# Performance work log

Hardware: AMD Instinct MI355X
Metric: run time of the kernel (lower is better)

The kernel has to match this reference:

```python
import jax, jax.numpy as jnp
import numpy as np

N_VOX = 500000
P, S, K = 2048, 64, 8          # pixels(rays), samples per ray, voxel neighbors per sample
F_M, F_H = 64, 128             # voxel feature dim, mlp hidden dim
FREQ_PE = 4
DEPTH_MIN, DEPTH_MAX = 1.0, 80.0
RAY_SAMPLE_STEPS = 64.0
EPS = 1e-10
IN_FEAT = F_M + 3 * FREQ_PE * 2  # 88


def lrelu(x):
    return jnp.where(x >= 0, x, 0.1 * x)  # LeakyReLU(0.1)


def posenc(x, L=FREQ_PE):
    # NeRF positional encoding: sin/cos(2^i * x), i in [0, L)
    freqs = 2.0 ** jnp.arange(L, dtype=x.dtype)          # [L]
    ang = x[..., None] * freqs                            # [..., 3, L]
    enc = jnp.concatenate([jnp.sin(ang), jnp.cos(ang)], axis=-1)  # [..., 3, 2L]
    return enc.reshape(x.shape[:-1] + (x.shape[-1] * 2 * L,))


def setup_inputs() -> dict:
    key = jax.random.key(0)
    ks = jax.random.split(key, 16)

    def xavier(k, fan_in, fan_out):
        return jax.random.normal(k, (fan_in, fan_out), jnp.float32) / np.sqrt(fan_in)

    inp = {
        'map_xyz': jax.random.normal(ks[0], (N_VOX, 3), jnp.float32),
        'map_feat': jax.random.normal(ks[1], (N_VOX, F_M), jnp.float32) * 0.05,
        'ind_voxel': jax.random.randint(ks[2], (P, S, K), 0, N_VOX),
        'sample_xyz': jax.random.normal(ks[3], (P, S, 3), jnp.float32),
        'dist_to_cam': jax.random.uniform(ks[4], (P, S), jnp.float32) * RAY_SAMPLE_STEPS,
        'W0': xavier(ks[5], IN_FEAT, F_H), 'b0': jnp.full((F_H,), 0.01, jnp.float32),
        'W1': xavier(ks[6], F_H, F_H),     'b1': jnp.full((F_H,), 0.01, jnp.float32),
        'W2': xavier(ks[7], F_H, F_H),     'b2': jnp.full((F_H,), 0.01, jnp.float32),
        'Wa0': xavier(ks[8], F_H, F_H // 2), 'ba0': jnp.full((F_H // 2,), 0.01, jnp.float32),
        'Wa1': xavier(ks[9], F_H // 2, 1),   'ba1': jnp.full((1,), 0.01, jnp.float32),
        'Wr0': xavier(ks[10], F_H, F_H // 2), 'br0': jnp.full((F_H // 2,), 0.01, jnp.float32),
        'Wr1': xavier(ks[11], F_H // 2, 3),   'br1': jnp.full((3,), 0.01, jnp.float32),
    }
    return inp


def reference(map_xyz, map_feat, ind_voxel, sample_xyz, dist_to_cam,
              W0, b0, W1, b1, W2, b2, Wa0, ba0, Wa1, ba1, Wr0, br0, Wr1, br1):
    # ---- voxel -> sample messages (func_msg_voxel_to_sample) ----
    voxel_xyz = map_xyz[ind_voxel]                       # [P,S,K,3] gather
    feat = map_feat[ind_voxel]                           # [P,S,K,F_M] gather
    offset = sample_xyz[:, :, None, :] - voxel_xyz       # [P,S,K,3]
    h = jnp.concatenate([feat, posenc(offset)], axis=-1) # [P,S,K,88]
    h = lrelu(h @ W0 + b0)
    h = lrelu(h @ W1 + b1)
    h = lrelu(h @ W2 + b2)                               # [P,S,K,F_H]
    w = jnp.exp(-10.0 * jnp.linalg.norm(offset, axis=-1))  # [P,S,K]
    w = w / jnp.sum(w, axis=-1, keepdims=True)
    # ---- reduce over K neighbors (func_reduce_voxel_to_sample) ----
    feat_s = jnp.sum(h * w[..., None], axis=2)           # [P,S,F_H]
    a = lrelu(feat_s @ Wa0 + ba0)
    alpha = jax.nn.sigmoid(a @ Wa1 + ba1)                # [P,S,1]
    r = lrelu(feat_s @ Wr0 + br0)
    rgb = jax.nn.sigmoid(r @ Wr1 + br1)                  # [P,S,3]
    # ---- sample -> pixel volume rendering (func_reduce_sample_to_pixel) ----
    dist = DEPTH_MIN + DEPTH_MAX * dist_to_cam / RAY_SAMPLE_STEPS  # [P,S]
    ones = jnp.ones((P, 1, 1), alpha.dtype)
    trans = jnp.cumprod(jnp.concatenate([ones, 1.0 - alpha + EPS], axis=1), axis=1)[:, :-1, :]
    blend = alpha * trans                                # [P,S,1]
    pixel_rgb = jnp.sum(rgb * blend, axis=1)             # [P,3]
    pixel_d = jnp.sum(dist[..., None] * blend, axis=1)   # [P,1]
    acc = jnp.sum(blend, axis=1)                         # [P,1]
    return jnp.concatenate([pixel_rgb, pixel_d, acc], axis=-1)  # [P,5]
```

## Files before the change

kernel.cpp:

```cpp
#include <hip/hip_runtime.h>

typedef __bf16 bf16_t;
typedef __bf16 bf16x2 __attribute__((ext_vector_type(2)));
typedef __bf16 bf16x4 __attribute__((ext_vector_type(4)));
typedef __bf16 bf16x8 __attribute__((ext_vector_type(8)));
typedef float  f32x4  __attribute__((ext_vector_type(4)));

#define NPIX 2048
#define NS   64
#define NK   8
#define NSAMP (NPIX*NS)
#define NROWS (NSAMP*NK)
#define TROWS 64
#define NTILES (NROWS/TROWS)
#define XSTR 104
#define HSTR 136

#define PK_W0 0
#define PK_W1 1536
#define PK_W2 3584
#define PK_WA 5632
#define PK_WR 6656
#define PK_TOT 7680

#define WS_AR_BYTES 122880

__global__ void pack_weights(const float* __restrict__ W0, const float* __restrict__ W1,
                             const float* __restrict__ W2, const float* __restrict__ Wa0,
                             const float* __restrict__ Wr0, bf16_t* __restrict__ dst0) {
  int tid = blockIdx.x * blockDim.x + threadIdx.x;
  if (tid >= PK_TOT * 8) return;
  const float* src; bf16_t* dst; int e, KD, ND, KS;
  if (tid < 12288)      { src = W0;  dst = dst0;         e = tid;         KD = 88;  ND = 128; KS = 3; }
  else if (tid < 28672) { src = W1;  dst = dst0 + 12288; e = tid - 12288; KD = 128; ND = 128; KS = 4; }
  else if (tid < 45056) { src = W2;  dst = dst0 + 28672; e = tid - 28672; KD = 128; ND = 128; KS = 4; }
  else if (tid < 53248) { src = Wa0; dst = dst0 + 45056; e = tid - 45056; KD = 128; ND = 64;  KS = 4; }
  else                  { src = Wr0; dst = dst0 + 53248; e = tid - 53248; KD = 128; ND = 64;  KS = 4; }
  int j = e & 7, l = (e >> 3) & 63, f = e >> 9;
  int s = f % KS, t = f / KS;
  int row = s * 32 + (l >> 4) * 8 + j;
  int col = t * 16 + (l & 15);
  float v = (row < KD) ? src[row * ND + col] : 0.f;
  dst[e] = (bf16_t)v;
}

__device__ __forceinline__ float lrelu(float v) { return fmaxf(v, 0.1f * v); }
__device__ __forceinline__ float sigmoidf(float x) { return 1.f / (1.f + __expf(-x)); }

__global__ __launch_bounds__(512, 4)
void nerf_main(const float* __restrict__ map_xyz, const float* __restrict__ map_feat,
               const int* __restrict__ ind, const float* __restrict__ sample_xyz,
               const float* __restrict__ b0g, const float* __restrict__ b1g,
               const float* __restrict__ b2g, const float* __restrict__ ba0g,
               const float* __restrict__ wa1g, const float* __restrict__ ba1g,
               const float* __restrict__ br0g, const float* __restrict__ wr1g,
               const float* __restrict__ br1g, const bf16_t* __restrict__ wpack,
               float* __restrict__ ar_out)
{
  __shared__ __align__(16) bf16_t sBuf[TROWS * HSTR];
  __shared__ __align__(16) bf16_t sHa[TROWS * HSTR];
  __shared__ __align__(16) bf16_t sFS[16 * HSTR];
  __shared__ __align__(16) bf16_t sAR[16 * HSTR];
  __shared__ __align__(16) bf16_t sFB[2048];
  __shared__ __align__(16) float sWt[TROWS];
  __shared__ float sWs[8];
  __shared__ __align__(16) float sB0[128], sB1[128], sB2[128], sBH[128], sFBv[4];

  const int tid = threadIdx.x;
  const int wid = tid >> 6, l = tid & 63;
  const int q = l >> 4, n = l & 15;
  const int sr = tid >> 3, sp = tid & 7;

  const bf16x8* pk = (const bf16x8*)wpack;
  bf16x8 w0f[3], w1f[4], w2f[4], hdf[4];
#pragma unroll
  for (int s = 0; s < 3; s++) w0f[s] = pk[PK_W0 + (wid * 3 + s) * 64 + l];
#pragma unroll
  for (int s = 0; s < 4; s++) w1f[s] = pk[PK_W1 + (wid * 4 + s) * 64 + l];
#pragma unroll
  for (int s = 0; s < 4; s++) w2f[s] = pk[PK_W2 + (wid * 4 + s) * 64 + l];
#pragma unroll
  for (int s = 0; s < 4; s++)
    hdf[s] = pk[(wid < 4 ? PK_WA : PK_WR) + ((wid & 3) * 4 + s) * 64 + l];

  for (int i = tid; i < 8 * HSTR; i += 512) {
    sFS[8 * HSTR + i] = (bf16_t)0.f;
    sAR[8 * HSTR + i] = (bf16_t)0.f;
  }
  {
    int e0 = tid * 4;
    int jb = e0 & 7, ll = (e0 >> 3) & 63, s = e0 >> 9;
    int m = ll & 15;
#pragma unroll
    for (int ii = 0; ii < 4; ii++) {
      int k = s * 32 + (ll >> 4) * 8 + jb + ii;
      float v = 0.f;
      if (k < 64)  { if (m < 3) v = wr1g[k * 3 + m]; }
      else         { if (m == 3) v = wa1g[k - 64]; }
      sFB[e0 + ii] = (bf16_t)v;
    }
  }
  if (tid < 128)      sB0[tid] = b0g[tid];
  else if (tid < 256) sB1[tid - 128] = b1g[tid - 128];
  else if (tid < 384) sB2[tid - 256] = b2g[tid - 256];
  else { int t = tid - 384; sBH[t] = (t < 64) ? ba0g[t] : br0g[t - 64]; }
  if (tid < 4) sFBv[tid] = (tid < 3) ? br1g[tid] : ba1g[0];
  __syncthreads();

  int   pidx = 0;
  float4 pf0 = {}, pf1 = {};
  float ps0 = 0.f, ps1 = 0.f, ps2 = 0.f, pm0 = 0.f, pm1 = 0.f, pm2 = 0.f;

  auto prefetch = [&](int t) {
    const int m = t * TROWS + sr;
    pidx = ind[m];
    const float4* fp = (const float4*)(map_feat + (size_t)pidx * 64 + sp * 8);
    pf0 = fp[0]; pf1 = fp[1];
    const int g = m >> 3;
    if (sp < 6) {
      const int d = sp >> 1;
      ps0 = sample_xyz[g * 3 + d];
      pm0 = map_xyz[pidx * 3 + d];
    } else if (sp == 7) {
      ps0 = sample_xyz[g * 3 + 0]; pm0 = map_xyz[pidx * 3 + 0];
      ps1 = sample_xyz[g * 3 + 1]; pm1 = map_xyz[pidx * 3 + 1];
      ps2 = sample_xyz[g * 3 + 2]; pm2 = map_xyz[pidx * 3 + 2];
    }
  };

  prefetch(blockIdx.x);

  for (int tile = blockIdx.x; tile < NTILES; tile += gridDim.x) {
    const int m0 = tile * TROWS;

    {
      bf16x8 v;
      v[0] = (bf16_t)pf0.x; v[1] = (bf16_t)pf0.y; v[2] = (bf16_t)pf0.z; v[3] = (bf16_t)pf0.w;
      v[4] = (bf16_t)pf1.x; v[5] = (bf16_t)pf1.y; v[6] = (bf16_t)pf1.z; v[7] = (bf16_t)pf1.w;
      *(bf16x8*)(sBuf + sr * XSTR + sp * 8) = v;
      if (sp < 6) {
        const int d = sp >> 1;
        float o = ps0 - pm0;
        float s1 = __sinf(o), c1 = __cosf(o);
        float s2 = 2.f * s1 * c1, c2 = 1.f - 2.f * s1 * s1;
        float s4 = 2.f * s2 * c2, c4 = 1.f - 2.f * s2 * s2;
        float s8 = 2.f * s4 * c4, c8 = 1.f - 2.f * s4 * s4;
        bf16x4 e;
        if (sp & 1) { e[0] = (bf16_t)c1; e[1] = (bf16_t)c2; e[2] = (bf16_t)c4; e[3] = (bf16_t)c8; }
        else        { e[0] = (bf16_t)s1; e[1] = (bf16_t)s2; e[2] = (bf16_t)s4; e[3] = (bf16_t)s8; }
        *(bf16x4*)(sBuf + sr * XSTR + 64 + d * 8 + (sp & 1) * 4) = e;
      } else if (sp == 6) {
        bf16x8 z = {};
        *(bf16x8*)(sBuf + sr * XSTR + 88) = z;
      } else {
        float ox = ps0 - pm0, oy = ps1 - pm1, oz = ps2 - pm2;
        sWt[sr] = __expf(-10.f * sqrtf(ox * ox + oy * oy + oz * oz));
      }
    }
    __syncthreads();

    {
      int nt = tile + (int)gridDim.x;
      if (nt < NTILES) prefetch(nt);
    }

    if (tid < 8) {
      float ss = 0.f;
#pragma unroll
      for (int k = 0; k < 8; k++) ss += sWt[tid * 8 + k];
      sWs[tid] = ss;
    }

    {
      f32x4 b0i = *(const f32x4*)(sB0 + wid * 16 + q * 4);
      f32x4 acc[4] = {b0i, b0i, b0i, b0i};
      __builtin_amdgcn_s_setprio(1);
#pragma unroll
      for (int st = 0; st < 4; st++)
#pragma unroll
        for (int s = 0; s < 3; s++) {
          bf16x8 b = *(const bf16x8*)(sBuf + (st * 16 + n) * XSTR + s * 32 + q * 8);
          acc[st] = __builtin_amdgcn_mfma_f32_16x16x32_bf16(w0f[s], b, acc[st], 0, 0, 0);
        }
      __builtin_amdgcn_s_setprio(0);
#pragma unroll
      for (int st = 0; st < 4; st++) {
        bf16x4 o;
        o[0] = (bf16_t)lrelu(acc[st][0]);
        o[1] = (bf16_t)lrelu(acc[st][1]);
        o[2] = (bf16_t)lrelu(acc[st][2]);
        o[3] = (bf16_t)lrelu(acc[st][3]);
        *(bf16x4*)(sHa + (st * 16 + n) * HSTR + wid * 16 + q * 4) = o;
      }
    }
    __syncthreads();

    {
      f32x4 b1i = *(const f32x4*)(sB1 + wid * 16 + q * 4);
      f32x4 acc[4] = {b1i, b1i, b1i, b1i};
      __builtin_amdgcn_s_setprio(1);
#pragma unroll
      for (int st = 0; st < 4; st++)
#pragma unroll
        for (int s = 0; s < 4; s++) {
          bf16x8 b = *(const bf16x8*)(sHa + (st * 16 + n) * HSTR + s * 32 + q * 8);
          acc[st] = __builtin_amdgcn_mfma_f32_16x16x32_bf16(w1f[s], b, acc[st], 0, 0, 0);
        }
      __builtin_amdgcn_s_setprio(0);
#pragma unroll
      for (int st = 0; st < 4; st++) {
        bf16x4 o;
        o[0] = (bf16_t)lrelu(acc[st][0]);
        o[1] = (bf16_t)lrelu(acc[st][1]);
        o[2] = (bf16_t)lrelu(acc[st][2]);
        o[3] = (bf16_t)lrelu(acc[st][3]);
        *(bf16x4*)(sBuf + (st * 16 + n) * HSTR + wid * 16 + q * 4) = o;
      }
    }
    __syncthreads();

    {
      f32x4 b2i = *(const f32x4*)(sB2 + wid * 16 + q * 4);
      f32x4 acc[4] = {b2i, b2i, b2i, b2i};
      __builtin_amdgcn_s_setprio(1);
#pragma unroll
      for (int st = 0; st < 4; st++)
#pragma unroll
        for (int s = 0; s < 4; s++) {
          bf16x8 b = *(const bf16x8*)(sBuf + (st * 16 + n) * HSTR + s * 32 + q * 8);
          acc[st] = __builtin_amdgcn_mfma_f32_16x16x32_bf16(w2f[s], b, acc[st], 0, 0, 0);
        }
      __builtin_amdgcn_s_setprio(0);
#pragma unroll
      for (int st = 0; st < 4; st++) {
        bf16x4 o;
        o[0] = (bf16_t)lrelu(acc[st][0]);
        o[1] = (bf16_t)lrelu(acc[st][1]);
        o[2] = (bf16_t)lrelu(acc[st][2]);
        o[3] = (bf16_t)lrelu(acc[st][3]);
        *(bf16x4*)(sHa + (st * 16 + n) * HSTR + wid * 16 + q * 4) = o;
      }
    }
    __syncthreads();

    {
      int g = tid >> 6;
      int c = (tid & 63) * 2;
      float a0 = 0.f, a1 = 0.f;
#pragma unroll
      for (int k = 0; k < 8; k++) {
        float wk = sWt[g * 8 + k];
        unsigned u = *(const unsigned*)(sHa + (g * 8 + k) * HSTR + c);
        a0 += wk * __uint_as_float(u << 16);
        a1 += wk * __uint_as_float(u & 0xffff0000u);
      }
      float inv = 1.f / sWs[g];
      bf16x2 fo;
      fo[0] = (bf16_t)(a0 * inv);
      fo[1] = (bf16_t)(a1 * inv);
      *(bf16x2*)(sFS + g * HSTR + c) = fo;
    }
    __syncthreads();

    {
      f32x4 ha = *(const f32x4*)(sBH + wid * 16 + q * 4);
      __builtin_amdgcn_s_setprio(1);
#pragma unroll
      for (int s = 0; s < 4; s++) {
        bf16x8 b = *(const bf16x8*)(sFS + n * HSTR + s * 32 + q * 8);
        ha = __builtin_amdgcn_mfma_f32_16x16x32_bf16(hdf[s], b, ha, 0, 0, 0);
      }
      __builtin_amdgcn_s_setprio(0);
      if (n < 8) {
        const int base = (wid < 4) ? 64 : 0;
        bf16x4 o;
        o[0] = (bf16_t)lrelu(ha[0]);
        o[1] = (bf16_t)lrelu(ha[1]);
        o[2] = (bf16_t)lrelu(ha[2]);
        o[3] = (bf16_t)lrelu(ha[3]);
        *(bf16x4*)(sAR + n * HSTR + base + (wid & 3) * 16 + q * 4) = o;
      }
    }
    __syncthreads();

    if (wid == 0) {
      f32x4 c = *(const f32x4*)sFBv;
#pragma unroll
      for (int s = 0; s < 4; s++) {
        bf16x8 a = *(const bf16x8*)(sFB + (s * 64 + l) * 8);
        bf16x8 b = *(const bf16x8*)(sAR + n * HSTR + s * 32 + q * 8);
        c = __builtin_amdgcn_mfma_f32_16x16x32_bf16(a, b, c, 0, 0, 0);
      }
      if (q == 0 && n < 8) {
        float4 o;
        o.x = sigmoidf(c[0]);
        o.y = sigmoidf(c[1]);
        o.z = sigmoidf(c[2]);
        o.w = sigmoidf(c[3]);
        ((float4*)ar_out)[m0 / 8 + n] = o;
      }
    }
  }
}

__global__ __launch_bounds__(512)
void render_kernel(const float* __restrict__ ar, const float* __restrict__ dcam,
                   float* __restrict__ out) {
  int ray = blockIdx.x * 8 + (threadIdx.x >> 6);
  int s = threadIdx.x & 63;
  float4 v = ((const float4*)ar)[ray * 64 + s];
  float alpha = v.w;
  float t = 1.f - alpha + 1e-10f;
  float p = t;
#pragma unroll
  for (int d = 1; d < 64; d <<= 1) {
    float o = __shfl_up(p, d);
    if (s >= d) p *= o;
  }
  float pm1 = __shfl_up(p, 1);
  float T = (s == 0) ? 1.f : pm1;
  float bl = alpha * T;
  float dist = 1.f + 1.25f * dcam[ray * 64 + s];
  float cr = v.x * bl, cg = v.y * bl, cb = v.z * bl, cd = dist * bl, ca = bl;
#pragma unroll
  for (int d = 32; d > 0; d >>= 1) {
    cr += __shfl_xor(cr, d);
    cg += __shfl_xor(cg, d);
    cb += __shfl_xor(cb, d);
    cd += __shfl_xor(cd, d);
    ca += __shfl_xor(ca, d);
  }
  if (s == 0) {
    out[ray * 5 + 0] = cr; out[ray * 5 + 1] = cg; out[ray * 5 + 2] = cb;
    out[ray * 5 + 3] = cd; out[ray * 5 + 4] = ca;
  }
}

extern "C" void kernel_launch(void* const* d_in, const int* in_sizes, int n_in,
                              void* d_out, int out_size, void* d_ws, size_t ws_size,
                              hipStream_t stream) {
  const float* map_xyz    = (const float*)d_in[0];
  const float* map_feat   = (const float*)d_in[1];
  const int*   ind        = (const int*)d_in[2];
  const float* sample_xyz = (const float*)d_in[3];
  const float* dist_cam   = (const float*)d_in[4];
  const float* W0  = (const float*)d_in[5];
  const float* b0  = (const float*)d_in[6];
  const float* W1  = (const float*)d_in[7];
  const float* b1  = (const float*)d_in[8];
  const float* W2  = (const float*)d_in[9];
  const float* b2  = (const float*)d_in[10];
  const float* Wa0 = (const float*)d_in[11];
  const float* ba0 = (const float*)d_in[12];
  const float* Wa1 = (const float*)d_in[13];
  const float* ba1 = (const float*)d_in[14];
  const float* Wr0 = (const float*)d_in[15];
  const float* br0 = (const float*)d_in[16];
  const float* Wr1 = (const float*)d_in[17];
  const float* br1 = (const float*)d_in[18];

  bf16_t* wpack = (bf16_t*)d_ws;
  float*  ar    = (float*)((char*)d_ws + WS_AR_BYTES);

  pack_weights<<<240, 256, 0, stream>>>(W0, W1, W2, Wa0, Wr0, wpack);
  nerf_main<<<512, 512, 0, stream>>>(map_xyz, map_feat, ind, sample_xyz,
                                     b0, b1, b2, ba0, Wa1, ba1, br0, Wr1, br1,
                                     wpack, ar);
  render_kernel<<<256, 512, 0, stream>>>(ar, dist_cam, (float*)d_out);
}
```

Measured before the change: 409.9 us.

## Prefetch gathered voxel features directly into LDS with async global_load_lds

Replaces the register-held prefetch of the next tile's voxel features and coordinates with global_load_lds writes into new swizzled LDS buffers (sFeat, sVxyz, sSxyz). The index loads are issued early in the loop and the DMA-style copies after the barrier, so the gathers overlap with the MLP compute without occupying VGPRs. The cost is about 17 KB of extra LDS per block, which may limit occupancy. The LDS write ordering also relies on later barriers and the implicit vmcnt waits being correct.

```diff
diff --git a/kernel.cpp b/kernel.cpp
--- a/kernel.cpp
+++ b/kernel.cpp
@@ -24,6 +24,10 @@
 #define PK_TOT 7680
 
 #define WS_AR_BYTES 122880
+
+#define GLDS16(g, s) __builtin_amdgcn_global_load_lds(                          \
+    (const __attribute__((address_space(1))) void*)(g),                         \
+    (__attribute__((address_space(3))) void*)(s), 16, 0, 0)
 
 __global__ void pack_weights(const float* __restrict__ W0, const float* __restrict__ W1,
                              const float* __restrict__ W2, const float* __restrict__ Wa0,
@@ -65,6 +69,9 @@
   __shared__ __align__(16) float sWt[TROWS];
   __shared__ float sWs[8];
   __shared__ __align__(16) float sB0[128], sB1[128], sB2[128], sBH[128], sFBv[4];
+  __shared__ __align__(16) float sFeat[64 * 64];
+  __shared__ __align__(16) float sVxyz[64 * 4];
+  __shared__ __align__(16) float sSxyz[32];
 
   const int tid = threadIdx.x;
   const int wid = tid >> 6, l = tid & 63;
@@ -82,6 +89,24 @@
 #pragma unroll
   for (int s = 0; s < 4; s++)
     hdf[s] = pk[(wid < 4 ? PK_WA : PK_WR) + ((wid & 3) * 4 + s) * 64 + l];
+
+  int pidxA = 0, pidxB = 0, pidxC = 0;
+  float sampv = 0.f;
+  auto issueA = [&](int nt) {
+    const int m0n = nt * TROWS;
+    pidxA = ind[m0n + wid * 8 + (l >> 4)];
+    pidxB = ind[m0n + wid * 8 + 4 + (l >> 4)];
+    if (wid == 0) pidxC = ind[m0n + l];
+    if (wid == 1 && l < 24) sampv = sample_xyz[nt * 24 + l];
+  };
+  auto issueB = [&]() {
+    const int ca = (l & 15) ^ (l >> 4);
+    const int cb = (l & 15) ^ (4 | (l >> 4));
+    GLDS16(map_feat + (size_t)pidxA * 64 + ca * 4, sFeat + wid * 512);
+    GLDS16(map_feat + (size_t)pidxB * 64 + cb * 4, sFeat + wid * 512 + 256);
+    if (wid == 0) GLDS16(map_xyz + (size_t)pidxC * 3, sVxyz);
+    if (wid == 1 && l < 24) sSxyz[l] = sampv;
+  };
 
   for (int i = tid; i < 8 * HSTR; i += 512) {
     sFS[8 * HSTR + i] = (bf16_t)0.f;
@@ -105,42 +130,29 @@
   else if (tid < 384) sB2[tid - 256] = b2g[tid - 256];
   else { int t = tid - 384; sBH[t] = (t < 64) ? ba0g[t] : br0g[t - 64]; }
   if (tid < 4) sFBv[tid] = (tid < 3) ? br1g[tid] : ba1g[0];
+
+  issueA(blockIdx.x);
+  issueB();
   __syncthreads();
-
-  int   pidx = 0;
-  float4 pf0 = {}, pf1 = {};
-  float ps0 = 0.f, ps1 = 0.f, ps2 = 0.f, pm0 = 0.f, pm1 = 0.f, pm2 = 0.f;
-
-  auto prefetch = [&](int t) {
-    const int m = t * TROWS + sr;
-    pidx = ind[m];
-    const float4* fp = (const float4*)(map_feat + (size_t)pidx * 64 + sp * 8);
-    pf0 = fp[0]; pf1 = fp[1];
-    const int g = m >> 3;
-    if (sp < 6) {
-      const int d = sp >> 1;
-      ps0 = sample_xyz[g * 3 + d];
-      pm0 = map_xyz[pidx * 3 + d];
-    } else if (sp == 7) {
-      ps0 = sample_xyz[g * 3 + 0]; pm0 = map_xyz[pidx * 3 + 0];
-      ps1 = sample_xyz[g * 3 + 1]; pm1 = map_xyz[pidx * 3 + 1];
-      ps2 = sample_xyz[g * 3 + 2]; pm2 = map_xyz[pidx * 3 + 2];
-    }
-  };
-
-  prefetch(blockIdx.x);
 
   for (int tile = blockIdx.x; tile < NTILES; tile += gridDim.x) {
     const int m0 = tile * TROWS;
-
-    {
+    const int nt = tile + (int)gridDim.x;
+
+    if (nt < NTILES) issueA(nt);
+
+    {
+      const int sw = sr & 7;
+      const float* fb = sFeat + sr * 64;
+      f32x4 lo = *(const f32x4*)(fb + (((2 * sp)     ^ sw) << 2));
+      f32x4 hi = *(const f32x4*)(fb + (((2 * sp + 1) ^ sw) << 2));
       bf16x8 v;
-      v[0] = (bf16_t)pf0.x; v[1] = (bf16_t)pf0.y; v[2] = (bf16_t)pf0.z; v[3] = (bf16_t)pf0.w;
-      v[4] = (bf16_t)pf1.x; v[5] = (bf16_t)pf1.y; v[6] = (bf16_t)pf1.z; v[7] = (bf16_t)pf1.w;
+      v[0] = (bf16_t)lo[0]; v[1] = (bf16_t)lo[1]; v[2] = (bf16_t)lo[2]; v[3] = (bf16_t)lo[3];
+      v[4] = (bf16_t)hi[0]; v[5] = (bf16_t)hi[1]; v[6] = (bf16_t)hi[2]; v[7] = (bf16_t)hi[3];
       *(bf16x8*)(sBuf + sr * XSTR + sp * 8) = v;
       if (sp < 6) {
         const int d = sp >> 1;
-        float o = ps0 - pm0;
+        float o = sSxyz[(sr >> 3) * 3 + d] - sVxyz[sr * 4 + d];
         float s1 = __sinf(o), c1 = __cosf(o);
         float s2 = 2.f * s1 * c1, c2 = 1.f - 2.f * s1 * s1;
         float s4 = 2.f * s2 * c2, c4 = 1.f - 2.f * s2 * s2;
@@ -153,16 +165,15 @@
         bf16x8 z = {};
         *(bf16x8*)(sBuf + sr * XSTR + 88) = z;
       } else {
-        float ox = ps0 - pm0, oy = ps1 - pm1, oz = ps2 - pm2;
+        float ox = sSxyz[(sr >> 3) * 3 + 0] - sVxyz[sr * 4 + 0];
+        float oy = sSxyz[(sr >> 3) * 3 + 1] - sVxyz[sr * 4 + 1];
+        float oz = sSxyz[(sr >> 3) * 3 + 2] - sVxyz[sr * 4 + 2];
         sWt[sr] = __expf(-10.f * sqrtf(ox * ox + oy * oy + oz * oz));
       }
     }
     __syncthreads();
 
-    {
-      int nt = tile + (int)gridDim.x;
-      if (nt < NTILES) prefetch(nt);
-    }
+    if (nt < NTILES) issueB();
 
     if (tid < 8) {
       float ss = 0.f;
```

Result: faster. 396.5 us (-3.3%).

## Software-pipeline two tiles per iteration to interleave MLP stages and cut barriers

Applied to the files above, without the earlier changes.

The per-block tile loop is restructured so two tiles (A and B) are in flight at once: gather/encode, layer 0, layers 1 and 2, the K-reduction, the heads and the final outputs of one tile run in the same barrier phase as different stages of the other tile. This cuts the number of block-wide barriers per tile and lets MFMA work overlap the global gathers. The old register prefetch of the next tile's features is dropped; gathers are now issued inline and hidden only by the other tile's compute. Grid size and iteration count are hard-coded, and the extra LDS buffers raise shared-memory use per block, which may lower occupancy.

```diff
diff --git a/kernel.cpp b/kernel.cpp
--- a/kernel.cpp
+++ b/kernel.cpp
@@ -13,6 +13,8 @@
 #define NROWS (NSAMP*NK)
 #define TROWS 64
 #define NTILES (NROWS/TROWS)
+#define GRID   512
+#define NIT    16
 #define XSTR 104
 #define HSTR 136
 
@@ -57,13 +59,14 @@
                const float* __restrict__ br1g, const bf16_t* __restrict__ wpack,
                float* __restrict__ ar_out)
 {
-  __shared__ __align__(16) bf16_t sBuf[TROWS * HSTR];
-  __shared__ __align__(16) bf16_t sHa[TROWS * HSTR];
+  __shared__ __align__(16) bf16_t sH0[TROWS * HSTR];
+  __shared__ __align__(16) bf16_t sH1[TROWS * HSTR];
+  __shared__ __align__(16) bf16_t sX[TROWS * XSTR];
   __shared__ __align__(16) bf16_t sFS[16 * HSTR];
   __shared__ __align__(16) bf16_t sAR[16 * HSTR];
   __shared__ __align__(16) bf16_t sFB[2048];
-  __shared__ __align__(16) float sWt[TROWS];
-  __shared__ float sWs[8];
+  __shared__ __align__(16) float sWtA[TROWS], sWtB[TROWS];
+  __shared__ float sWsA[8], sWsB[8];
   __shared__ __align__(16) float sB0[128], sB1[128], sB2[128], sBH[128], sFBv[4];
 
   const int tid = threadIdx.x;
@@ -83,206 +86,123 @@
   for (int s = 0; s < 4; s++)
     hdf[s] = pk[(wid < 4 ? PK_WA : PK_WR) + ((wid & 3) * 4 + s) * 64 + l];
 
-  for (int i = tid; i < 8 * HSTR; i += 512) {
-    sFS[8 * HSTR + i] = (bf16_t)0.f;
-    sAR[8 * HSTR + i] = (bf16_t)0.f;
-  }
-  {
-    int e0 = tid * 4;
-    int jb = e0 & 7, ll = (e0 >> 3) & 63, s = e0 >> 9;
-    int m = ll & 15;
-#pragma unroll
-    for (int ii = 0; ii < 4; ii++) {
-      int k = s * 32 + (ll >> 4) * 8 + jb + ii;
-      float v = 0.f;
-      if (k < 64)  { if (m < 3) v = wr1g[k * 3 + m]; }
-      else         { if (m == 3) v = wa1g[k - 64]; }
-      sFB[e0 + ii] = (bf16_t)v;
-    }
-  }
-  if (tid < 128)      sB0[tid] = b0g[tid];
-  else if (tid < 256) sB1[tid - 128] = b1g[tid - 128];
-  else if (tid < 384) sB2[tid - 256] = b2g[tid - 256];
-  else { int t = tid - 384; sBH[t] = (t < 64) ? ba0g[t] : br0g[t - 64]; }
-  if (tid < 4) sFBv[tid] = (tid < 3) ? br1g[tid] : ba1g[0];
-  __syncthreads();
-
-  int   pidx = 0;
-  float4 pf0 = {}, pf1 = {};
-  float ps0 = 0.f, ps1 = 0.f, ps2 = 0.f, pm0 = 0.f, pm1 = 0.f, pm2 = 0.f;
-
-  auto prefetch = [&](int t) {
-    const int m = t * TROWS + sr;
-    pidx = ind[m];
-    const float4* fp = (const float4*)(map_feat + (size_t)pidx * 64 + sp * 8);
-    pf0 = fp[0]; pf1 = fp[1];
+  auto COMMIT = [&](int tile, bf16_t* X, float* wtbuf) {
+    const int m = tile * TROWS + sr;
+    const int idx = ind[m];
+    const float4* fp = (const float4*)(map_feat + (size_t)idx * 64 + sp * 8);
+    float4 f0 = fp[0], f1 = fp[1];
+    bf16x8 v;
+    v[0] = (bf16_t)f0.x; v[1] = (bf16_t)f0.y; v[2] = (bf16_t)f0.z; v[3] = (bf16_t)f0.w;
+    v[4] = (bf16_t)f1.x; v[5] = (bf16_t)f1.y; v[6] = (bf16_t)f1.z; v[7] = (bf16_t)f1.w;
+    *(bf16x8*)(X + sr * XSTR + sp * 8) = v;
     const int g = m >> 3;
     if (sp < 6) {
       const int d = sp >> 1;
-      ps0 = sample_xyz[g * 3 + d];
-      pm0 = map_xyz[pidx * 3 + d];
-    } else if (sp == 7) {
-      ps0 = sample_xyz[g * 3 + 0]; pm0 = map_xyz[pidx * 3 + 0];
-      ps1 = sample_xyz[g * 3 + 1]; pm1 = map_xyz[pidx * 3 + 1];
-      ps2 = sample_xyz[g * 3 + 2]; pm2 = map_xyz[pidx * 3 + 2];
-    }
-  };
-
-  prefetch(blockIdx.x);
-
-  for (int tile = blockIdx.x; tile < NTILES; tile += gridDim.x) {
-    const int m0 = tile * TROWS;
-
-    {
-      bf16x8 v;
-      v[0] = (bf16_t)pf0.x; v[1] = (bf16_t)pf0.y; v[2] = (bf16_t)pf0.z; v[3] = (bf16_t)pf0.w;
-      v[4] = (bf16_t)pf1.x; v[5] = (bf16_t)pf1.y; v[6] = (bf16_t)pf1.z; v[7] = (bf16_t)pf1.w;
-      *(bf16x8*)(sBuf + sr * XSTR + sp * 8) = v;
-      if (sp < 6) {
-        const int d = sp >> 1;
-        float o = ps0 - pm0;
-        float s1 = __sinf(o), c1 = __cosf(o);
-        float s2 = 2.f * s1 * c1, c2 = 1.f - 2.f * s1 * s1;
-        float s4 = 2.f * s2 * c2, c4 = 1.f - 2.f * s2 * s2;
-        float s8 = 2.f * s4 * c4, c8 = 1.f - 2.f * s4 * s4;
-        bf16x4 e;
-        if (sp & 1) { e[0] = (bf16_t)c1; e[1] = (bf16_t)c2; e[2] = (bf16_t)c4; e[3] = (bf16_t)c8; }
-        else        { e[0] = (bf16_t)s1; e[1] = (bf16_t)s2; e[2] = (bf16_t)s4; e[3] = (bf16_t)s8; }
-        *(bf16x4*)(sBuf + sr * XSTR + 64 + d * 8 + (sp & 1) * 4) = e;
-      } else if (sp == 6) {
-        bf16x8 z = {};
-        *(bf16x8*)(sBuf + sr * XSTR + 88) = z;
-      } else {
-        float ox = ps0 - pm0, oy = ps1 - pm1, oz = ps2 - pm2;
-        sWt[sr] = __expf(-10.f * sqrtf(ox * ox + oy * oy + oz * oz));
+      float o = sample_xyz[g * 3 + d] - map_xyz[idx * 3 + d];
+      float s1 = __sinf(o), c1 = __cosf(o);
+      float s2 = 2.f * s1 * c1, c2 = 1.f - 2.f * s1 * s1;
+      float s4 = 2.f * s2 * c2, c4 = 1.f - 2.f * s2 * s2;
+      float s8 = 2.f * s4 * c4, c8 = 1.f - 2.f * s4 * s4;
+      bf16x4 e;
+      if (sp & 1) { e[0] = (bf16_t)c1; e[1] = (bf16_t)c2; e[2] = (bf16_t)c4; e[3] = (bf16_t)c8; }
+      else        { e[0] = (bf16_t)s1; e[1] = (bf16_t)s2; e[2] = (bf16_t)s4; e[3] = (bf16_t)s8; }
+      *(bf16x4*)(X + sr * XSTR + 64 + d * 8 + (sp & 1) * 4) = e;
+    } else if (sp == 6) {
+      bf16x8 z = {};
+      *(bf16x8*)(X + sr * XSTR + 88) = z;
+    } else {
+      float ox = sample_xyz[g * 3 + 0] - map_xyz[idx * 3 + 0];
+      float oy = sample_xyz[g * 3 + 1] - map_xyz[idx * 3 + 1];
+      float oz = sample_xyz[g * 3 + 2] - map_xyz[idx * 3 + 2];
+      wtbuf[sr] = __expf(-10.f * sqrtf(ox * ox + oy * oy + oz * oz));
+    }
+  };
+
+  auto L0 = [&](const bf16_t* X, bf16_t* Hout) {
+    f32x4 bi = *(const f32x4*)(sB0 + wid * 16 + q * 4);
+    f32x4 acc[4] = {bi, bi, bi, bi};
+    __builtin_amdgcn_s_setprio(1);
+#pragma unroll
+    for (int st = 0; st < 4; st++)
+#pragma unroll
+      for (int s = 0; s < 3; s++) {
+        bf16x8 b = *(const bf16x8*)(X + (st * 16 + n) * XSTR + s * 32 + q * 8);
+        acc[st] = __builtin_amdgcn_mfma_f32_16x16x32_bf16(w0f[s], b, acc[st], 0, 0, 0);
       }
-    }
-    __syncthreads();
-
-    {
-      int nt = tile + (int)gridDim.x;
-      if (nt < NTILES) prefetch(nt);
-    }
-
-    if (tid < 8) {
-      float ss = 0.f;
-#pragma unroll
-      for (int k = 0; k < 8; k++) ss += sWt[tid * 8 + k];
-      sWs[tid] = ss;
-    }
-
-    {
-      f32x4 b0i = *(const f32x4*)(sB0 + wid * 16 + q * 4);
-      f32x4 acc[4] = {b0i, b0i, b0i, b0i};
-      __builtin_amdgcn_s_setprio(1);
-#pragma unroll
-      for (int st = 0; st < 4; st++)
-#pragma unroll
-        for (int s = 0; s < 3; s++) {
-          bf16x8 b = *(const bf16x8*)(sBuf + (st * 16 + n) * XSTR + s * 32 + q * 8);
-          acc[st] = __builtin_amdgcn_mfma_f32_16x16x32_bf16(w0f[s], b, acc[st], 0, 0, 0);
-        }
-      __builtin_amdgcn_s_setprio(0);
-#pragma unroll
-      for (int st = 0; st < 4; st++) {
-        bf16x4 o;
-        o[0] = (bf16_t)lrelu(acc[st][0]);
-        o[1] = (bf16_t)lrelu(acc[st][1]);
-        o[2] = (bf16_t)lrelu(acc[st][2]);
-        o[3] = (bf16_t)lrelu(acc[st][3]);
-        *(bf16x4*)(sHa + (st * 16 + n) * HSTR + wid * 16 + q * 4) = o;
+    __builtin_amdgcn_s_setprio(0);
+#pragma unroll
+    for (int st = 0; st < 4; st++) {
+      bf16x4 o;
+      o[0] = (bf16_t)lrelu(acc[st][0]);
+      o[1] = (bf16_t)lrelu(acc[st][1]);
+      o[2] = (bf16_t)lrelu(acc[st][2]);
+      o[3] = (bf16_t)lrelu(acc[st][3]);
+      *(bf16x4*)(Hout + (st * 16 + n) * HSTR + wid * 16 + q * 4) = o;
+    }
+  };
+
+  auto LAYER = [&](const bf16_t* Hin, bf16_t* Hout, const bf16x8* wf, const float* bg) {
+    f32x4 bi = *(const f32x4*)(bg + wid * 16 + q * 4);
+    f32x4 acc[4] = {bi, bi, bi, bi};
+    __builtin_amdgcn_s_setprio(1);
+#pragma unroll
+    for (int st = 0; st < 4; st++)
+#pragma unroll
+      for (int s = 0; s < 4; s++) {
+        bf16x8 b = *(const bf16x8*)(Hin + (st * 16 + n) * HSTR + s * 32 + q * 8);
+        acc[st] = __builtin_amdgcn_mfma_f32_16x16x32_bf16(wf[s], b, acc[st], 0, 0, 0);
       }
-    }
-    __syncthreads();
-
-    {
-      f32x4 b1i = *(const f32x4*)(sB1 + wid * 16 + q * 4);
-      f32x4 acc[4] = {b1i, b1i, b1i, b1i};
-      __builtin_amdgcn_s_setprio(1);
-#pragma unroll
-      for (int st = 0; st < 4; st++)
-#pragma unroll
-        for (int s = 0; s < 4; s++) {
-          bf16x8 b = *(const bf16x8*)(sHa + (st * 16 + n) * HSTR + s * 32 + q * 8);
-          acc[st] = __builtin_amdgcn_mfma_f32_16x16x32_bf16(w1f[s], b, acc[st], 0, 0, 0);
-        }
-      __builtin_amdgcn_s_setprio(0);
-#pragma unroll
-      for (int st = 0; st < 4; st++) {
-        bf16x4 o;
-        o[0] = (bf16_t)lrelu(acc[st][0]);
-        o[1] = (bf16_t)lrelu(acc[st][1]);
-        o[2] = (bf16_t)lrelu(acc[st][2]);
-        o[3] = (bf16_t)lrelu(acc[st][3]);
-        *(bf16x4*)(sBuf + (st * 16 + n) * HSTR + wid * 16 + q * 4) = o;
-      }
-    }
-    __syncthreads();
-
-    {
-      f32x4 b2i = *(const f32x4*)(sB2 + wid * 16 + q * 4);
-      f32x4 acc[4] = {b2i, b2i, b2i, b2i};
-      __builtin_amdgcn_s_setprio(1);
-#pragma unroll
-      for (int st = 0; st < 4; st++)
-#pragma unroll
-        for (int s = 0; s < 4; s++) {
-          bf16x8 b = *(const bf16x8*)(sBuf + (st * 16 + n) * HSTR + s * 32 + q * 8);
-          acc[st] = __builtin_amdgcn_mfma_f32_16x16x32_bf16(w2f[s], b, acc[st], 0, 0, 0);
-        }
-      __builtin_amdgcn_s_setprio(0);
-#pragma unroll
-      for (int st = 0; st < 4; st++) {
-        bf16x4 o;
-        o[0] = (bf16_t)lrelu(acc[st][0]);
-        o[1] = (bf16_t)lrelu(acc[st][1]);
-        o[2] = (bf16_t)lrelu(acc[st][2]);
-        o[3] = (bf16_t)lrelu(acc[st][3]);
-        *(bf16x4*)(sHa + (st * 16 + n) * HSTR + wid * 16 + q * 4) = o;
-      }
-    }
-    __syncthreads();
-
-    {
-      int g = tid >> 6;
-      int c = (tid & 63) * 2;
-      float a0 = 0.f, a1 = 0.f;
-#pragma unroll
-      for (int k = 0; k < 8; k++) {
-        float wk = sWt[g * 8 + k];
-        unsigned u = *(const unsigned*)(sHa + (g * 8 + k) * HSTR + c);
-        a0 += wk * __uint_as_float(u << 16);
-        a1 += wk * __uint_as_float(u & 0xffff0000u);
-      }
-      float inv = 1.f / sWs[g];
-      bf16x2 fo;
-      fo[0] = (bf16_t)(a0 * inv);
-      fo[1] = (bf16_t)(a1 * inv);
-      *(bf16x2*)(sFS + g * HSTR + c) = fo;
-    }
-    __syncthreads();
-
-    {
-      f32x4 ha = *(const f32x4*)(sBH + wid * 16 + q * 4);
-      __builtin_amdgcn_s_setprio(1);
-#pragma unroll
-      for (int s = 0; s < 4; s++) {
-        bf16x8 b = *(const bf16x8*)(sFS + n * HSTR + s * 32 + q * 8);
-        ha = __builtin_amdgcn_mfma_f32_16x16x32_bf16(hdf[s], b, ha, 0, 0, 0);
-      }
-      __builtin_amdgcn_s_setprio(0);
-      if (n < 8) {
-        const int base = (wid < 4) ? 64 : 0;
-        bf16x4 o;
-        o[0] = (bf16_t)lrelu(ha[0]);
-        o[1] = (bf16_t)lrelu(ha[1]);
-        o[2] = (bf16_t)lrelu(ha[2]);
-        o[3] = (bf16_t)lrelu(ha[3]);
-        *(bf16x4*)(sAR + n * HSTR + base + (wid & 3) * 16 + q * 4) = o;
-      }
-    }
-    __syncthreads();
-
+    __builtin_amdgcn_s_setprio(0);
+#pragma unroll
+    for (int st = 0; st < 4; st++) {
+      bf16x4 o;
+      o[0] = (bf16_t)lrelu(acc[st][0]);
+      o[1] = (bf16_t)lrelu(acc[st][1]);
+      o[2] = (bf16_t)lrelu(acc[st][2]);
+      o[3] = (bf16_t)lrelu(acc[st][3]);
+      *(bf16x4*)(Hout + (st * 16 + n) * HSTR + wid * 16 + q * 4) = o;
+    }
+  };
+
+  auto KRED = [&](const bf16_t* Hin, const float* wt, const float* ws, bf16_t* FS) {
+    int g = tid >> 6;
+    int c = (tid & 63) * 2;
+    float a0 = 0.f, a1 = 0.f;
+#pragma unroll
+    for (int k = 0; k < 8; k++) {
+      float wk = wt[g * 8 + k];
+      unsigned u = *(const unsigned*)(Hin + (g * 8 + k) * HSTR + c);
+      a0 += wk * __uint_as_float(u << 16);
+      a1 += wk * __uint_as_float(u & 0xffff0000u);
+    }
+    float inv = 1.f / ws[g];
+    bf16x2 fo;
+    fo[0] = (bf16_t)(a0 * inv);
+    fo[1] = (bf16_t)(a1 * inv);
+    *(bf16x2*)(FS + g * HSTR + c) = fo;
+  };
+
+  auto HEADS = [&](const bf16_t* FS, bf16_t* AR) {
+    f32x4 ha = *(const f32x4*)(sBH + wid * 16 + q * 4);
+    __builtin_amdgcn_s_setprio(1);
+#pragma unroll
+    for (int s = 0; s < 4; s++) {
+      bf16x8 b = *(const bf16x8*)(FS + n * HSTR + s * 32 + q * 8);
+      ha = __builtin_amdgcn_mfma_f32_16x16x32_bf16(hdf[s], b, ha, 0, 0, 0);
+    }
+    __builtin_amdgcn_s_setprio(0);
+    if (n < 8) {
+      const int base = (wid < 4) ? 64 : 0;
+      bf16x4 o;
+      o[0] = (bf16_t)lrelu(ha[0]);
+      o[1] = (bf16_t)lrelu(ha[1]);
+      o[2] = (bf16_t)lrelu(ha[2]);
+      o[3] = (bf16_t)lrelu(ha[3]);
+      *(bf16x4*)(AR + n * HSTR + base + (wid & 3) * 16 + q * 4) = o;
+    }
+  };
+
+  auto FINALS = [&](int tile) {
     if (wid == 0) {
       f32x4 c = *(const f32x4*)sFBv;
 #pragma unroll
@@ -297,9 +217,82 @@
         o.y = sigmoidf(c[1]);
         o.z = sigmoidf(c[2]);
         o.w = sigmoidf(c[3]);
-        ((float4*)ar_out)[m0 / 8 + n] = o;
+        ((float4*)ar_out)[tile * 8 + n] = o;
       }
     }
+  };
+
+  for (int i = tid; i < 8 * HSTR; i += 512) {
+    sFS[8 * HSTR + i] = (bf16_t)0.f;
+    sAR[8 * HSTR + i] = (bf16_t)0.f;
+  }
+  {
+    int e0 = tid * 4;
+    int jb = e0 & 7, ll = (e0 >> 3) & 63, s = e0 >> 9;
+    int m = ll & 15;
+#pragma unroll
+    for (int ii = 0; ii < 4; ii++) {
+      int k = s * 32 + (ll >> 4) * 8 + jb + ii;
+      float v = 0.f;
+      if (k < 64)  { if (m < 3) v = wr1g[k * 3 + m]; }
+      else         { if (m == 3) v = wa1g[k - 64]; }
+      sFB[e0 + ii] = (bf16_t)v;
+    }
+  }
+  if (tid < 128)      sB0[tid] = b0g[tid];
+  else if (tid < 256) sB1[tid - 128] = b1g[tid - 128];
+  else if (tid < 384) sB2[tid - 256] = b2g[tid - 256];
+  else { int t = tid - 384; sBH[t] = (t < 64) ? ba0g[t] : br0g[t - 64]; }
+  if (tid < 4) sFBv[tid] = (tid < 3) ? br1g[tid] : ba1g[0];
+  __syncthreads();
+
+  for (int it = 0; it <= NIT; ++it) {
+    const bool a_on = (it < NIT);
+    const bool b_on = (it > 0);
+    const int tA  = (int)blockIdx.x + (2 * it) * GRID;
+    const int tAp = (int)blockIdx.x + (2 * it - 2) * GRID;
+    const int tB  = (int)blockIdx.x + (2 * it + 1) * GRID;
+    const int tBp = (int)blockIdx.x + (2 * it - 1) * GRID;
+
+    if (a_on) COMMIT(tA, sX, sWtA);
+    if (b_on) LAYER(sH0, sH1, w2f, sB2);
+    if (b_on) FINALS(tAp);
+    __syncthreads();
+
+    if (a_on) L0(sX, sH0);
+    if (b_on) KRED(sH1, sWtB, sWsB, sFS);
+    if (a_on && tid < 8) {
+      float ss = 0.f;
+#pragma unroll
+      for (int k = 0; k < 8; k++) ss += sWtA[tid * 8 + k];
+      sWsA[tid] = ss;
+    }
+    __syncthreads();
+
+    if (a_on) LAYER(sH0, sH1, w1f, sB1);
+    if (b_on) HEADS(sFS, sAR);
+    __syncthreads();
+
+    if (a_on) COMMIT(tB, sX, sWtB);
+    if (a_on) LAYER(sH1, sH0, w2f, sB2);
+    if (b_on) FINALS(tBp);
+    __syncthreads();
+
+    if (it == NIT) break;
+
+    L0(sX, sH1);
+    KRED(sH0, sWtA, sWsA, sFS);
+    if (tid < 8) {
+      float ss = 0.f;
+#pragma unroll
+      for (int k = 0; k < 8; k++) ss += sWtB[tid * 8 + k];
+      sWsB[tid] = ss;
+    }
+    __syncthreads();
+
+    LAYER(sH1, sH0, w1f, sB1);
+    HEADS(sFS, sAR);
+    __syncthreads();
   }
 }
 
@@ -363,8 +356,8 @@
   float*  ar    = (float*)((char*)d_ws + WS_AR_BYTES);
 
   pack_weights<<<240, 256, 0, stream>>>(W0, W1, W2, Wa0, Wr0, wpack);
-  nerf_main<<<512, 512, 0, stream>>>(map_xyz, map_feat, ind, sample_xyz,
-                                     b0, b1, b2, ba0, Wa1, ba1, br0, Wr1, br1,
-                                     wpack, ar);
+  nerf_main<<<GRID, 512, 0, stream>>>(map_xyz, map_feat, ind, sample_xyz,
+                                      b0, b1, b2, ba0, Wa1, ba1, br0, Wr1, br1,
+                                      wpack, ar);
   render_kernel<<<256, 512, 0, stream>>>(ar, dist_cam, (float*)d_out);
 }
```

Measured after the change: 393.9 us. -3.9%, faster.
